# Kernel tuning notes

Measured on AMD Instinct MI355X. Metric: run time of the kernel, lower is better.

The kernel has to match this reference:

```python
import jax, jax.numpy as jnp
import numpy as np
from jax import lax

B, N, D = 4, 64, 32  # graphs, nodes/graph, volume side
HC = 1024            # hidden_channels
NF = 2048            # num_node_features = 32*(D//8)**3
NC = 4               # num_classes
LC = 256             # linear_channels = N*(HC//4)//64


def setup_inputs() -> dict:
    key = jax.random.key(0)
    ks = jax.random.split(key, 16)
    x = jax.random.normal(ks[0], (B, N, D, D, D), jnp.float32)
    # binary symmetric adjacency, zero diagonal (edge presence only; GCNConv ignores values)
    u = jax.random.uniform(ks[1], (B, N, N))
    a = (u < 0.2).astype(jnp.int32)
    a = jnp.maximum(a, a.transpose(0, 2, 1)) * (1 - jnp.eye(N, dtype=jnp.int32))
    s = 0.05
    inp = dict(
        x=x, adj=a, batch_size=B,
        w_conv1=jax.random.normal(ks[2], (16, 1, 3, 3, 3), jnp.float32) * s,
        b_conv1=jnp.zeros((16,), jnp.float32),
        w_conv2=jax.random.normal(ks[3], (32, 16, 3, 3, 3), jnp.float32) * s,
        b_conv2=jnp.zeros((32,), jnp.float32),
        w_g1=jax.random.normal(ks[4], (NF, HC), jnp.float32) * s,
        b_g1=jnp.zeros((HC,), jnp.float32),
        w_g2=jax.random.normal(ks[5], (HC, HC // 2), jnp.float32) * s,
        b_g2=jnp.zeros((HC // 2,), jnp.float32),
        w_g3=jax.random.normal(ks[6], (HC // 2, HC // 4), jnp.float32) * s,
        b_g3=jnp.zeros((HC // 4,), jnp.float32),
        w_fc1=jax.random.normal(ks[7], (LC, 2 * LC), jnp.float32) * s,
        b_fc1=jnp.zeros((2 * LC,), jnp.float32),
        w_fc2=jax.random.normal(ks[8], (2 * LC, NC), jnp.float32) * s,
        b_fc2=jnp.zeros((NC,), jnp.float32),
    )
    return inp


DN = ('NCDHW', 'OIDHW', 'NCDHW')


def _maxpool3(h):
    # MaxPool3d(kernel=3, stride=2, padding=1); pad value -inf matches torch
    return lax.reduce_window(h, -jnp.inf, lax.max,
                             (1, 1, 3, 3, 3), (1, 1, 2, 2, 2),
                             [(0, 0), (0, 0), (1, 1), (1, 1), (1, 1)])


def _gcn_norm(adj, dtype):
    # GCNConv: A_hat = A + I, sym-normalized D^-1/2 A_hat D^-1/2 (per graph)
    A = (adj != 0).astype(dtype) + jnp.eye(adj.shape[-1], dtype=dtype)[None]
    deg = A.sum(-1)                        # [B, N], >= 1
    dinv = deg ** -0.5
    return A * dinv[:, :, None] * dinv[:, None, :]


def _forward(x, adj, batch_size, w_conv1, b_conv1, w_conv2, b_conv2,
             w_g1, b_g1, w_g2, b_g2, w_g3, b_g3, w_fc1, b_fc1, w_fc2, b_fc2):
    b, n = x.shape[0], x.shape[1]
    v = x.reshape(b * n, 1, x.shape[2], x.shape[3], x.shape[4])
    h = lax.conv_general_dilated(v, w_conv1, (1, 1, 1), [(1, 1)] * 3, dimension_numbers=DN)
    h = jax.nn.relu(h + b_conv1[None, :, None, None, None])
    h = _maxpool3(h)                                     # [BN,16,16,16,16]
    h = lax.conv_general_dilated(h, w_conv2, (2, 2, 2), [(1, 1)] * 3, dimension_numbers=DN)
    h = jax.nn.relu(h + b_conv2[None, :, None, None, None])
    h = _maxpool3(h)                                     # [BN,32,4,4,4]
    feat = h.reshape(b, n, -1)                           # [B,N,2048]

    A_norm = _gcn_norm(adj, feat.dtype)                  # [B,N,N]
    gcn = lambda X, W, bb: jnp.einsum('bij,bjf->bif', A_norm, X @ W) + bb
    g = jax.nn.relu(gcn(feat, w_g1, b_g1))
    g = jax.nn.relu(gcn(g, w_g2, b_g2))
    g = gcn(g, w_g3, b_g3)                               # [B,N,256] (no relu, matches source)

    g = g.reshape(batch_size, -1)                        # [B, 16384]
    g = g.reshape(batch_size, -1, 64).max(-1)            # MaxPool1d(64) on 2D input -> [B,256]
    g = jax.nn.relu(g @ w_fc1 + b_fc1)
    return jax.nn.softmax(g @ w_fc2 + b_fc2, axis=-1)


def reference(x, adj, batch_size, w_conv1, b_conv1, w_conv2, b_conv2,
              w_g1, b_g1, w_g2, b_g2, w_g3, b_g3, w_fc1, b_fc1, w_fc2, b_fc2):
    return _forward(x, adj, batch_size, w_conv1, b_conv1, w_conv2, b_conv2,
                    w_g1, b_g1, w_g2, b_g2, w_g3, b_g3, w_fc1, b_fc1, w_fc2, b_fc2)
```

## Files before the change

kernel.cpp:

```cpp
#include <hip/hip_runtime.h>

typedef unsigned short ushort_t;
typedef unsigned long long ull_t;
typedef __attribute__((ext_vector_type(8))) short bf16x8;
typedef __attribute__((ext_vector_type(4))) float f32x4;

static __device__ __forceinline__ unsigned short f2bf(float f) {
  unsigned u = __float_as_uint(f);
  u = (u + 0x7FFFu + ((u >> 16) & 1u)) >> 16;
  return (unsigned short)u;
}

static __device__ __forceinline__ f32x4 max4(f32x4 a, f32x4 b) {
  f32x4 r;
  r[0] = fmaxf(a[0], b[0]); r[1] = fmaxf(a[1], b[1]);
  r[2] = fmaxf(a[2], b[2]); r[3] = fmaxf(a[3], b[3]);
  return r;
}


__device__ __forceinline__ void prep_transpose(
    const float* __restrict__ W, ushort_t* __restrict__ out,
    int K, int N, int n0, int k0, int t, float (*tile)[33])
{
  const int tx = t & 31, ty = t >> 5;
#pragma unroll
  for (int i = 0; i < 4; ++i) {
    const int k = k0 + ty + i * 8;
    tile[ty + i * 8][tx] = W[(size_t)k * N + n0 + tx];
  }
  __syncthreads();
#pragma unroll
  for (int i = 0; i < 4; ++i) {
    const int n = n0 + ty + i * 8;
    out[(size_t)n * K + k0 + tx] = f2bf(tile[tx][ty + i * 8]);
  }
}

__global__ __launch_bounds__(256) void k_prep(
    const float* __restrict__ x, ushort_t* __restrict__ xb16,
    const float* __restrict__ w2, ushort_t* __restrict__ w2f,
    const float* __restrict__ wg1, ushort_t* __restrict__ wg1T,
    const float* __restrict__ wg2, ushort_t* __restrict__ wg2T,
    const float* __restrict__ wg3, ushort_t* __restrict__ wg3T,
    const int* __restrict__ adj, float* __restrict__ An)
{
  __shared__ float tile[32][33];
  __shared__ float dinv[64];
  __shared__ int part[256];
  int b = blockIdx.x;
  const int t = threadIdx.x;
  if (b < 8192) {
    const int tid = b * 256 + t;
    const float4 v = ((const float4*)x)[tid];
    const unsigned lo = (unsigned)f2bf(v.x) | ((unsigned)f2bf(v.y) << 16);
    const unsigned hi = (unsigned)f2bf(v.z) | ((unsigned)f2bf(v.w) << 16);
    ((uint2*)xb16)[tid] = make_uint2(lo, hi);
    return;
  }
  b -= 8192;
  if (b < 56) {
    const int tid = b * 256 + t;
    if (tid < 14336) {
      const int nt = tid / 7168, rem = tid % 7168;
      const int kk = rem / 512, rem2 = rem % 512;
      const int l = rem2 >> 3, j = rem2 & 7;
      const int n = nt * 16 + (l & 15);
      const int k = (l >> 4) * 8 + kk * 32 + j;
      float v = 0.f;
      if (k < 432) v = w2[n * 432 + k];
      w2f[tid] = f2bf(v);
    }
    return;
  }
  b -= 56;
  if (b < 2048) { prep_transpose(wg1, wg1T, 2048, 1024, (b & 31) << 5, (b >> 5) << 5, t, tile); return; }
  b -= 2048;
  if (b < 512)  { prep_transpose(wg2, wg2T, 1024, 512,  (b & 15) << 5, (b >> 4) << 5, t, tile); return; }
  b -= 512;
  if (b < 128)  { prep_transpose(wg3, wg3T, 512,  256,  (b & 7)  << 5, (b >> 3) << 5, t, tile); return; }
  b -= 128;
  {
    const int i = t >> 2, q = t & 3;
    const int* ab = adj + b * 4096 + i * 64 + q * 16;
    int d = 0;
#pragma unroll
    for (int j = 0; j < 16; ++j) d += (ab[j] != 0) ? 1 : 0;
    part[t] = d;
    __syncthreads();
    if (q == 0)
      dinv[i] = rsqrtf((float)(1 + part[t] + part[t + 1] + part[t + 2] + part[t + 3]));
    __syncthreads();
    for (int idx = t; idx < 4096; idx += 256) {
      const int ii = idx >> 6, jj = idx & 63;
      const float a = (ii == jj) ? 1.f : ((adj[b * 4096 + idx] != 0) ? 1.f : 0.f);
      An[b * 4096 + idx] = a * dinv[ii] * dinv[jj];
    }
  }
}

__global__ __launch_bounds__(256) void k_conv1_mfma(
    const ushort_t* __restrict__ xb16, const float* __restrict__ wc,
    const float* __restrict__ bc, ushort_t* __restrict__ h1)
{
  __shared__ ushort_t L[2 * 34 * 76];
  char* Lb = (char*)L;
  const int bn = blockIdx.x >> 3, zg = blockIdx.x & 7;
  const int t = threadIdx.x;
  const int w = t >> 6, l = t & 63;
  const int grp = l >> 4, m = l & 15, ch = l & 15;
  const float NINF = -1e30f;

  union { short s[8]; bf16x8 v; } uA, uB;
#pragma unroll
  for (int j = 0; j < 8; ++j) {
    const int k = grp * 8 + j;
    float wA = 0.f, wB = 0.f;
    if (k < 12) {
      const int dx = k >> 2, dz = k & 3;
      if (dz < 3) { wA = wc[ch*27 + dz*9 + 0 + dx]; wB = wc[ch*27 + dz*9 + 6 + dx]; }
    } else if (k >= 16 && k < 28) {
      const int kk = k - 16, dx = kk >> 2, dz = kk & 3;
      if (dz < 3) wA = wc[ch*27 + dz*9 + 3 + dx];
    }
    uA.s[j] = (short)f2bf(wA);
    uB.s[j] = (short)f2bf(wB);
  }

  int aX1[3], aX2[3];
#pragma unroll
  for (int s = 0; s < 3; ++s) {
    const int Q1 = 2*m + s + 2*(grp & 1);
    const int Q2 = Q1 + 1;
    aX1[s] = (Q1 & 1) * 5168 + (Q1 >> 1) * 8;
    aX2[s] = (Q2 & 1) * 5168 + (Q2 >> 1) * 8;
  }
  const int rsel = (grp >> 1) * 152;

  for (int u = t; u < 200; u += 256) {
    int addr;
    if (u < 72) {
      const int rr = (u < 36) ? 0 : 33;
      const int s = (u < 36) ? u : u - 36;
      const int pp = s / 18, slot = s - pp * 18;
      addr = pp * 5168 + rr * 152 + slot * 8;
    } else {
      const int v = u - 72;
      const int rr = 1 + (v >> 2);
      const int pp = (v >> 1) & 1;
      const int slot = (v & 1) * 17;
      addr = pp * 5168 + rr * 152 + slot * 8;
    }
    *(ull_t*)(Lb + addr) = 0ull;
  }

  f32x4 accZ[4][2];
#pragma unroll
  for (int j = 0; j < 4; ++j)
#pragma unroll
    for (int p = 0; p < 2; ++p) accZ[j][p] = (f32x4){NINF, NINF, NINF, NINF};

  const ushort_t* xb = xb16 + (size_t)bn * 32768;

#pragma unroll 1
  for (int ci = 0; ci < 5; ++ci) {
    const int cz = 4*zg - 1 + ci;
    if (cz < 0) continue;
    if (t < 128) {
      const int r = 1 + (t >> 2), g = t & 3;
      const ushort_t* xrow = xb + (r - 1) * 32 + g * 8;
      uint4 u0 = make_uint4(0u, 0u, 0u, 0u), u2 = make_uint4(0u, 0u, 0u, 0u);
      if (cz > 0)  u0 = *(const uint4*)(xrow + (cz - 1) * 1024);
      const uint4 u1 = *(const uint4*)(xrow + cz * 1024);
      if (cz < 31) u2 = *(const uint4*)(xrow + (cz + 1) * 1024);
      char* b0 = Lb + r * 152 + (4 * g + 1) * 8;
      char* b1 = Lb + 5168 + r * 152 + (4 * g + 1) * 8;
      const unsigned* p0 = (const unsigned*)&u0;
      const unsigned* p1 = (const unsigned*)&u1;
      const unsigned* p2 = (const unsigned*)&u2;
#pragma unroll
      for (int e = 0; e < 4; ++e) {
        const unsigned w0 = p0[e], w1 = p1[e], w2v = p2[e];
        const unsigned lo_e = (w0 & 0xFFFFu) | (w1 << 16);
        const unsigned hi_e = (w2v & 0xFFFFu);
        const unsigned lo_o = (w0 >> 16) | (w1 & 0xFFFF0000u);
        const unsigned hi_o = (w2v >> 16);
        *(ull_t*)(b0 + e * 8) = (ull_t)lo_e | ((ull_t)hi_e << 32);
        *(ull_t*)(b1 + e * 8) = (ull_t)lo_o | ((ull_t)hi_o << 32);
      }
    }
    __syncthreads();
    f32x4 accP0 = (f32x4){NINF, NINF, NINF, NINF};
    f32x4 accP1 = (f32x4){NINF, NINF, NINF, NINF};
#pragma unroll
    for (int yy = 0; yy < 9; ++yy) {
      if (yy == 0 && w == 0) continue;
      const int y = 8 * w - 1 + yy;
      const int rbA = y * 152 + rsel;
      const int rbB = (y + 2) * 152;
      f32x4 Cy;
#pragma unroll
      for (int s = 0; s < 3; ++s) {
        union { ull_t u[2]; bf16x8 v; } fA, fB;
        fA.u[0] = *(const ull_t*)(Lb + aX1[s] + rbA);
        fA.u[1] = *(const ull_t*)(Lb + aX2[s] + rbA);
        fB.u[0] = *(const ull_t*)(Lb + aX1[s] + rbB);
        fB.u[1] = *(const ull_t*)(Lb + aX2[s] + rbB);
        f32x4 acc = (f32x4){0.f, 0.f, 0.f, 0.f};
        acc = __builtin_amdgcn_mfma_f32_16x16x32_bf16(fA.v, uA.v, acc, 0, 0, 0);
        acc = __builtin_amdgcn_mfma_f32_16x16x32_bf16(fB.v, uB.v, acc, 0, 0, 0);
        if (s == 0) acc[0] = (l < 16) ? NINF : acc[0];
        Cy = (s == 0) ? acc : max4(Cy, acc);
      }
      if (yy & 1) {
        const int c = (yy - 1) / 2;
        if ((c & 1) == 0) accP0 = max4(accP0, Cy); else accP1 = max4(accP1, Cy);
      } else {
        const int cl = yy / 2 - 1;
        const int chh = yy / 2;
        if (cl >= 0) {
          if ((cl & 1) == 0) {
            accP0 = max4(accP0, Cy);
            if (ci <= 2) accZ[cl][0] = max4(accZ[cl][0], accP0);
            if (ci >= 2) accZ[cl][1] = max4(accZ[cl][1], accP0);
            accP0 = (f32x4){NINF, NINF, NINF, NINF};
          } else {
            accP1 = max4(accP1, Cy);
            if (ci <= 2) accZ[cl][0] = max4(accZ[cl][0], accP1);
            if (ci >= 2) accZ[cl][1] = max4(accZ[cl][1], accP1);
            accP1 = (f32x4){NINF, NINF, NINF, NINF};
          }
        }
        if (chh <= 3) {
          if ((chh & 1) == 0) accP0 = max4(accP0, Cy); else accP1 = max4(accP1, Cy);
        }
      }
    }
    __syncthreads();
  }

  const float biasv = bc[ch];
#pragma unroll
  for (int j = 0; j < 4; ++j) {
    const int py = 4 * w + j;
#pragma unroll
    for (int p = 0; p < 2; ++p) {
      const int pz = 2 * zg + p;
      const f32x4 v = accZ[j][p];
      const unsigned lo = (unsigned)f2bf(fmaxf(v[0] + biasv, 0.f)) |
                          ((unsigned)f2bf(fmaxf(v[1] + biasv, 0.f)) << 16);
      const unsigned hi = (unsigned)f2bf(fmaxf(v[2] + biasv, 0.f)) |
                          ((unsigned)f2bf(fmaxf(v[3] + biasv, 0.f)) << 16);
      ushort_t* dst = h1 + (((size_t)(bn * 16 + ch) * 16 + pz) << 8) + py * 16 + grp * 4;
      *(uint2*)dst = make_uint2(lo, hi);
    }
  }
}

__global__ __launch_bounds__(128) void k_conv2(
    const ushort_t* __restrict__ h1, const ushort_t* __restrict__ w2f,
    float* __restrict__ c2)
{
  __shared__ ushort_t U[16 * 456];
  ushort_t* Hs = U;
  unsigned* Hsd = (unsigned*)U;
  ushort_t* As = U;
  const int b = blockIdx.x;
  const int bn = b >> 5, oz = (b >> 2) & 7, yg = b & 3;
  const int t = threadIdx.x;
  const ushort_t* hb = h1 + ((size_t)bn << 16);
  const int w = t >> 6, l = t & 63;

  bf16x8 bfr[14];
#pragma unroll
  for (int kk = 0; kk < 14; ++kk)
    bfr[kk] = *(const bf16x8*)(const void*)&w2f[(((w * 14) + kk) * 64 + l) * 8];

#pragma unroll
  for (int it = 0; it < 9; ++it) {
    const int u = t + it * 128;
    const int row = u >> 2, q = u & 3;
    const int ic = row / 18;
    const int r2 = row - ic * 18;
    const int izp = r2 / 6;
    const int iyp = r2 - izp * 6;
    const int iz = 2 * oz - 1 + izp;
    const int iy = 4 * yg - 1 + iyp;
    uint2 v = make_uint2(0u, 0u);
    if ((unsigned)iz < 16u && (unsigned)iy < 16u)
      v = *(const uint2*)(hb + (ic << 12) + (iz << 8) + (iy << 4) + q * 4);
    *(uint2*)&Hs[row * 20 + q * 4] = v;
  }
  __syncthreads();

  const int m = t >> 3, sub = t & 7;
  const int ox = m & 7;
  const int my = (m >> 3) * 2;
  ushort_t tv[54];
  int j = 0;
#pragma unroll
  for (int ic2 = 0; ic2 < 2; ++ic2) {
    const int ic = sub * 2 + ic2;
#pragma unroll
    for (int dz = 0; dz < 3; ++dz) {
#pragma unroll
      for (int dy = 0; dy < 3; ++dy) {
        const int row = ic * 18 + dz * 6 + my + dy;
        const unsigned* rp = Hsd + row * 10;
        const unsigned d0 = (ox > 0) ? rp[ox - 1] : 0u;
        const unsigned d1 = rp[ox];
        tv[j]     = (ushort_t)(d0 >> 16);
        tv[j + 1] = (ushort_t)(d1 & 0xFFFFu);
        tv[j + 2] = (ushort_t)(d1 >> 16);
        j += 3;
      }
    }
  }
  __syncthreads();

  {
    unsigned* Aw = (unsigned*)As;
    const int wbase = m * 228 + sub * 27;
#pragma unroll
    for (int p = 0; p < 27; ++p)
      Aw[wbase + p] = (unsigned)tv[2 * p] | ((unsigned)tv[2 * p + 1] << 16);
    Aw[(t >> 3) * 228 + 216 + (t & 7)] = 0u;
  }
  __syncthreads();

  f32x4 acc = {0.f, 0.f, 0.f, 0.f};
  const ushort_t* arow = &As[(l & 15) * 456 + ((l >> 4) << 3)];
#pragma unroll
  for (int kk = 0; kk < 14; ++kk) {
    const bf16x8 af = *(const bf16x8*)(const void*)&arow[kk * 32];
    acc = __builtin_amdgcn_mfma_f32_16x16x32_bf16(af, bfr[kk], acc, 0, 0, 0);
  }
  const int n = w * 16 + (l & 15);
  const int m0 = (l >> 4) << 2;
  float* cb = c2 + (((size_t)(bn * 32 + n) * 8) + oz) * 64 + yg * 16 + m0;
  *(float4*)cb = make_float4(acc[0], acc[1], acc[2], acc[3]);
}

__global__ __launch_bounds__(256) void k_pool2(
    const float* __restrict__ c2, const float* __restrict__ bc2,
    ushort_t* __restrict__ featb)
{
  const int tid = blockIdx.x * 256 + threadIdx.x;
  const int bn = tid >> 9, r = tid & 511;
  const int ch = r >> 4, pz = (r >> 2) & 3, py = r & 3;
  const float* base = c2 + ((size_t)(bn * 32 + ch) << 9);
  float m0 = -1e30f, m1 = -1e30f, m2 = -1e30f, m3 = -1e30f;
#pragma unroll
  for (int dz = 0; dz < 3; ++dz) {
    const int oz = 2 * pz - 1 + dz;
    if ((unsigned)oz >= 8u) continue;
#pragma unroll
    for (int dy = 0; dy < 3; ++dy) {
      const int oy = 2 * py - 1 + dy;
      if ((unsigned)oy >= 8u) continue;
      const float* row = base + (oz << 6) + (oy << 3);
      const float4 a = ((const float4*)row)[0];
      const float4 b = ((const float4*)row)[1];
      m0 = fmaxf(m0, fmaxf(a.x, a.y));
      m1 = fmaxf(m1, fmaxf(a.y, fmaxf(a.z, a.w)));
      m2 = fmaxf(m2, fmaxf(a.w, fmaxf(b.x, b.y)));
      m3 = fmaxf(m3, fmaxf(b.y, fmaxf(b.z, b.w)));
    }
  }
  const float bb = bc2[ch];
  const unsigned lo = (unsigned)f2bf(fmaxf(m0 + bb, 0.f)) |
                      ((unsigned)f2bf(fmaxf(m1 + bb, 0.f)) << 16);
  const unsigned hi = (unsigned)f2bf(fmaxf(m2 + bb, 0.f)) |
                      ((unsigned)f2bf(fmaxf(m3 + bb, 0.f)) << 16);
  *(uint2*)(featb + (size_t)bn * 2048 + r * 4) = make_uint2(lo, hi);
}

__global__ __launch_bounds__(256) void k_gcn_layer(
    const ushort_t* __restrict__ Xb, const ushort_t* __restrict__ WT,
    const float* __restrict__ bias, const float* __restrict__ An,
    ushort_t* __restrict__ Ob, float* __restrict__ Of, int K, int N, int relu)
{
  __shared__ ushort_t As[2][64 * 72];
  __shared__ ushort_t Bs[2][64 * 72];
  __shared__ ushort_t Ps[64 * 72];
  const int b = blockIdx.y, jb = blockIdx.x << 6;
  const int t = threadIdx.x, w = t >> 6, l = t & 63;
  const int r0 = t >> 3, kc0 = t & 7;
  const int lm = l & 15, lg = l >> 4;

  union { short s[8]; bf16x8 v; } afr[2];
  {
    const float* ap = An + b * 4096 + (16 * w + lm) * 64 + (lg << 3);
#pragma unroll
    for (int kc = 0; kc < 2; ++kc) {
      const float4 v0 = *(const float4*)(ap + kc * 32);
      const float4 v1 = *(const float4*)(ap + kc * 32 + 4);
      afr[kc].s[0] = (short)f2bf(v0.x); afr[kc].s[1] = (short)f2bf(v0.y);
      afr[kc].s[2] = (short)f2bf(v0.z); afr[kc].s[3] = (short)f2bf(v0.w);
      afr[kc].s[4] = (short)f2bf(v1.x); afr[kc].s[5] = (short)f2bf(v1.y);
      afr[kc].s[6] = (short)f2bf(v1.z); afr[kc].s[7] = (short)f2bf(v1.w);
    }
  }

  f32x4 acc[4];
#pragma unroll
  for (int nt = 0; nt < 4; ++nt) acc[nt] = (f32x4){0.f, 0.f, 0.f, 0.f};

  const ushort_t* arow0 = &Xb[(size_t)(b * 64 + r0) * K + kc0 * 8];
  const ushort_t* arow1 = &Xb[(size_t)(b * 64 + r0 + 32) * K + kc0 * 8];
  const ushort_t* brow0 = &WT[(size_t)(jb + r0) * K + kc0 * 8];
  const ushort_t* brow1 = &WT[(size_t)(jb + r0 + 32) * K + kc0 * 8];

  uint4 va0 = *(const uint4*)arow0;
  uint4 va1 = *(const uint4*)arow1;
  uint4 vb0 = *(const uint4*)brow0;
  uint4 vb1 = *(const uint4*)brow1;

  int buf = 0;
#pragma unroll 1
  for (int kt = 0; kt < K; kt += 64) {
    *(uint4*)&As[buf][r0 * 72 + kc0 * 8]        = va0;
    *(uint4*)&As[buf][(r0 + 32) * 72 + kc0 * 8] = va1;
    *(uint4*)&Bs[buf][r0 * 72 + kc0 * 8]        = vb0;
    *(uint4*)&Bs[buf][(r0 + 32) * 72 + kc0 * 8] = vb1;
    __syncthreads();
    if (kt + 64 < K) {
      va0 = *(const uint4*)(arow0 + kt + 64);
      va1 = *(const uint4*)(arow1 + kt + 64);
      vb0 = *(const uint4*)(brow0 + kt + 64);
      vb1 = *(const uint4*)(brow1 + kt + 64);
    }
#pragma unroll
    for (int ks = 0; ks < 2; ++ks) {
      const bf16x8 af = *(const bf16x8*)(const void*)
          &As[buf][(16 * w + lm) * 72 + ks * 32 + (lg << 3)];
#pragma unroll
      for (int nt = 0; nt < 4; ++nt) {
        const bf16x8 bf = *(const bf16x8*)(const void*)
            &Bs[buf][(nt * 16 + lm) * 72 + ks * 32 + (lg << 3)];
        acc[nt] = __builtin_amdgcn_mfma_f32_16x16x32_bf16(af, bf, acc[nt], 0, 0, 0);
      }
    }
    buf ^= 1;
  }

  __syncthreads();
  const int m0 = lg << 2;
#pragma unroll
  for (int nt = 0; nt < 4; ++nt) {
    const int n = nt * 16 + lm;
    const unsigned lo = (unsigned)f2bf(acc[nt][0]) | ((unsigned)f2bf(acc[nt][1]) << 16);
    const unsigned hi = (unsigned)f2bf(acc[nt][2]) | ((unsigned)f2bf(acc[nt][3]) << 16);
    *(uint2*)&Ps[n * 72 + 16 * w + m0] = make_uint2(lo, hi);
  }
  __syncthreads();

#pragma unroll
  for (int nt = 0; nt < 4; ++nt) {
    const bf16x8 b0 = *(const bf16x8*)(const void*)&Ps[(nt * 16 + lm) * 72 + (lg << 3)];
    const bf16x8 b1 = *(const bf16x8*)(const void*)&Ps[(nt * 16 + lm) * 72 + 32 + (lg << 3)];
    f32x4 a2 = (f32x4){0.f, 0.f, 0.f, 0.f};
    a2 = __builtin_amdgcn_mfma_f32_16x16x32_bf16(afr[0].v, b0, a2, 0, 0, 0);
    a2 = __builtin_amdgcn_mfma_f32_16x16x32_bf16(afr[1].v, b1, a2, 0, 0, 0);
    const int col = jb + nt * 16 + lm;
    const float bv = bias[col];
#pragma unroll
    for (int r = 0; r < 4; ++r) {
      const int row = b * 64 + 16 * w + m0 + r;
      float v = a2[r] + bv;
      if (relu) v = fmaxf(v, 0.f);
      if (Ob) Ob[(size_t)row * N + col] = f2bf(v);
      else    Of[(size_t)row * N + col] = v;
    }
  }
}

__global__ __launch_bounds__(256) void k_head(
    const float* __restrict__ g3, const float* __restrict__ w1, const float* __restrict__ b1,
    const float* __restrict__ w2, const float* __restrict__ b2, float* __restrict__ out)
{
  const int b = blockIdx.x, t = threadIdx.x;
  __shared__ float sp[256];
  __shared__ float sh[512];
  __shared__ float sl[4];
  {
    const int n = t >> 2, c = t & 3;
    const float* gr = g3 + (size_t)(b * 64 + n) * 256 + c * 64;
    float mx = -1e30f;
    for (int f = 0; f < 64; ++f) mx = fmaxf(mx, gr[f]);
    sp[t] = mx;
  }
  __syncthreads();
  for (int jj = t; jj < 512; jj += 256) {
    float s = b1[jj];
    for (int k = 0; k < 256; ++k) s += sp[k] * w1[k * 512 + jj];
    sh[jj] = fmaxf(s, 0.f);
  }
  __syncthreads();
  if (t < 4) {
    float s = b2[t];
    for (int k = 0; k < 512; ++k) s += sh[k] * w2[k * 4 + t];
    sl[t] = s;
  }
  __syncthreads();
  if (t == 0) {
    const float mm = fmaxf(fmaxf(sl[0], sl[1]), fmaxf(sl[2], sl[3]));
    const float e0 = expf(sl[0] - mm), e1 = expf(sl[1] - mm);
    const float e2 = expf(sl[2] - mm), e3 = expf(sl[3] - mm);
    const float inv = 1.f / (e0 + e1 + e2 + e3);
    out[b * 4 + 0] = e0 * inv;
    out[b * 4 + 1] = e1 * inv;
    out[b * 4 + 2] = e2 * inv;
    out[b * 4 + 3] = e3 * inv;
  }
}

extern "C" void kernel_launch(void* const* d_in, const int* in_sizes, int n_in,
                              void* d_out, int out_size, void* d_ws, size_t ws_size,
                              hipStream_t stream)
{
  (void)in_sizes; (void)n_in; (void)out_size; (void)ws_size;
  const float* x   = (const float*)d_in[0];
  const int*   adj = (const int*)d_in[1];
  const float* wc1 = (const float*)d_in[3];
  const float* bc1 = (const float*)d_in[4];
  const float* wc2 = (const float*)d_in[5];
  const float* bc2 = (const float*)d_in[6];
  const float* wg1 = (const float*)d_in[7];
  const float* bg1 = (const float*)d_in[8];
  const float* wg2 = (const float*)d_in[9];
  const float* bg2 = (const float*)d_in[10];
  const float* wg3 = (const float*)d_in[11];
  const float* bg3 = (const float*)d_in[12];
  const float* wf1 = (const float*)d_in[13];
  const float* bf1 = (const float*)d_in[14];
  const float* wf2 = (const float*)d_in[15];
  const float* bf2 = (const float*)d_in[16];

  float* ws    = (float*)d_ws;
  ushort_t* h1 = (ushort_t*)d_ws;
  ushort_t* w2f   = (ushort_t*)(ws + 8388608);
  ushort_t* wg1Tb = (ushort_t*)(ws + 8395776);
  ushort_t* wg2Tb = (ushort_t*)(ws + 9444352);
  ushort_t* wg3Tb = (ushort_t*)(ws + 9706496);
  ushort_t* featb = (ushort_t*)(ws + 9772032);
  ushort_t* g1b   = (ushort_t*)(ws + 10034176);
  ushort_t* g2b   = (ushort_t*)(ws + 10165248);
  float* c2    = ws + 16777216;
  ushort_t* xb16 = (ushort_t*)(ws + 16777216);
  float* An   = ws + 21495808;
  float* g3   = ws + 22364160;
  float* outp = (float*)d_out;

  hipLaunchKernelGGL(k_prep,        dim3(10940),    dim3(256), 0, stream,
                     x, xb16, wc2, w2f, wg1, wg1Tb, wg2, wg2Tb, wg3, wg3Tb, adj, An);
  hipLaunchKernelGGL(k_conv1_mfma,  dim3(2048),     dim3(256), 0, stream, xb16, wc1, bc1, h1);
  hipLaunchKernelGGL(k_conv2,       dim3(8192),     dim3(128), 0, stream, h1, w2f, c2);
  hipLaunchKernelGGL(k_pool2,       dim3(512),      dim3(256), 0, stream, c2, bc2, featb);
  hipLaunchKernelGGL(k_gcn_layer,   dim3(16,4),     dim3(256), 0, stream,
                     featb, wg1Tb, bg1, An, g1b, (float*)nullptr, 2048, 1024, 1);
  hipLaunchKernelGGL(k_gcn_layer,   dim3(8,4),      dim3(256), 0, stream,
                     g1b, wg2Tb, bg2, An, g2b, (float*)nullptr, 1024, 512, 1);
  hipLaunchKernelGGL(k_gcn_layer,   dim3(4,4),      dim3(256), 0, stream,
                     g2b, wg3Tb, bg3, An, (ushort_t*)nullptr, g3, 512, 256, 0);
  hipLaunchKernelGGL(k_head,        dim3(4),        dim3(256), 0, stream, g3, wf1, bf1, wf2, bf2, outp);
}
```

Measured before the change: 268.9 us.

## Fuse GCN layers and head into one persistent kernel with grid barriers

```diff
diff --git a/kernel.cpp b/kernel.cpp
--- a/kernel.cpp
+++ b/kernel.cpp
@@ -16,6 +16,26 @@
   r[0] = fmaxf(a[0], b[0]); r[1] = fmaxf(a[1], b[1]);
   r[2] = fmaxf(a[2], b[2]); r[3] = fmaxf(a[3], b[3]);
   return r;
+}
+
+static __device__ __forceinline__ void gbar(int* bar, int nb) {
+  __syncthreads();
+  if (threadIdx.x == 0) {
+    const int g = atomicAdd(&bar[1], 0);
+    __threadfence();
+    if (atomicAdd(&bar[0], 1) == nb - 1) {
+      atomicExch(&bar[0], 0);
+      __threadfence();
+      atomicAdd(&bar[1], 1);
+    } else {
+      for (int it = 0; it < (1 << 24); ++it) {
+        if (atomicAdd(&bar[1], 0) != g) break;
+        __builtin_amdgcn_s_sleep(8);
+      }
+    }
+    __threadfence();
+  }
+  __syncthreads();
 }
 
 
@@ -343,8 +363,9 @@
 
 __global__ __launch_bounds__(256) void k_pool2(
     const float* __restrict__ c2, const float* __restrict__ bc2,
-    ushort_t* __restrict__ featb)
-{
+    ushort_t* __restrict__ featb, int* __restrict__ bar)
+{
+  if (blockIdx.x == 0 && threadIdx.x == 0) { bar[0] = 0; bar[1] = 0; }
   const int tid = blockIdx.x * 256 + threadIdx.x;
   const int bn = tid >> 9, r = tid & 511;
   const int ch = r >> 4, pz = (r >> 2) & 3, py = r & 3;
@@ -375,15 +396,13 @@
   *(uint2*)(featb + (size_t)bn * 2048 + r * 4) = make_uint2(lo, hi);
 }
 
-__global__ __launch_bounds__(256) void k_gcn_layer(
+__device__ __forceinline__ void gcn_body(
     const ushort_t* __restrict__ Xb, const ushort_t* __restrict__ WT,
     const float* __restrict__ bias, const float* __restrict__ An,
-    ushort_t* __restrict__ Ob, float* __restrict__ Of, int K, int N, int relu)
-{
-  __shared__ ushort_t As[2][64 * 72];
-  __shared__ ushort_t Bs[2][64 * 72];
-  __shared__ ushort_t Ps[64 * 72];
-  const int b = blockIdx.y, jb = blockIdx.x << 6;
+    ushort_t* __restrict__ Ob, float* __restrict__ spw,
+    int K, int N, int relu, int b, int jb,
+    ushort_t (*As)[64 * 72], ushort_t (*Bs)[64 * 72], ushort_t* Ps)
+{
   const int t = threadIdx.x, w = t >> 6, l = t & 63;
   const int r0 = t >> 3, kc0 = t & 7;
   const int lm = l & 15, lg = l >> 4;
@@ -455,6 +474,7 @@
   }
   __syncthreads();
 
+  float mx0 = -1e30f, mx1 = -1e30f, mx2 = -1e30f, mx3 = -1e30f;
 #pragma unroll
   for (int nt = 0; nt < 4; ++nt) {
     const bf16x8 b0 = *(const bf16x8*)(const void*)&Ps[(nt * 16 + lm) * 72 + (lg << 3)];
@@ -464,54 +484,126 @@
     a2 = __builtin_amdgcn_mfma_f32_16x16x32_bf16(afr[1].v, b1, a2, 0, 0, 0);
     const int col = jb + nt * 16 + lm;
     const float bv = bias[col];
-#pragma unroll
-    for (int r = 0; r < 4; ++r) {
-      const int row = b * 64 + 16 * w + m0 + r;
-      float v = a2[r] + bv;
-      if (relu) v = fmaxf(v, 0.f);
-      if (Ob) Ob[(size_t)row * N + col] = f2bf(v);
-      else    Of[(size_t)row * N + col] = v;
-    }
-  }
-}
-
-__global__ __launch_bounds__(256) void k_head(
-    const float* __restrict__ g3, const float* __restrict__ w1, const float* __restrict__ b1,
-    const float* __restrict__ w2, const float* __restrict__ b2, float* __restrict__ out)
-{
-  const int b = blockIdx.x, t = threadIdx.x;
-  __shared__ float sp[256];
-  __shared__ float sh[512];
-  __shared__ float sl[4];
+    if (spw) {
+      mx0 = fmaxf(mx0, a2[0] + bv);
+      mx1 = fmaxf(mx1, a2[1] + bv);
+      mx2 = fmaxf(mx2, a2[2] + bv);
+      mx3 = fmaxf(mx3, a2[3] + bv);
+    } else {
+#pragma unroll
+      for (int r = 0; r < 4; ++r) {
+        const int row = b * 64 + 16 * w + m0 + r;
+        float v = a2[r] + bv;
+        if (relu) v = fmaxf(v, 0.f);
+        Ob[(size_t)row * N + col] = f2bf(v);
+      }
+    }
+  }
+  if (spw) {
+#pragma unroll
+    for (int mk = 1; mk <= 8; mk <<= 1) {
+      mx0 = fmaxf(mx0, __shfl_xor(mx0, mk));
+      mx1 = fmaxf(mx1, __shfl_xor(mx1, mk));
+      mx2 = fmaxf(mx2, __shfl_xor(mx2, mk));
+      mx3 = fmaxf(mx3, __shfl_xor(mx3, mk));
+    }
+    if (lm == 0) {
+      const int c = jb >> 6;
+      const int n = 16 * w + m0;
+      spw[b * 256 + (n + 0) * 4 + c] = mx0;
+      spw[b * 256 + (n + 1) * 4 + c] = mx1;
+      spw[b * 256 + (n + 2) * 4 + c] = mx2;
+      spw[b * 256 + (n + 3) * 4 + c] = mx3;
+    }
+  }
+}
+
+__global__ __launch_bounds__(256) void k_tail(
+    const ushort_t* __restrict__ featb,
+    const ushort_t* __restrict__ wg1T, const float* __restrict__ bg1,
+    const ushort_t* __restrict__ wg2T, const float* __restrict__ bg2,
+    const ushort_t* __restrict__ wg3T, const float* __restrict__ bg3,
+    const float* __restrict__ An,
+    ushort_t* __restrict__ g1b, ushort_t* __restrict__ g2b,
+    float* __restrict__ spw, float* __restrict__ shw,
+    const float* __restrict__ w1, const float* __restrict__ b1,
+    const float* __restrict__ w2, const float* __restrict__ b2,
+    float* __restrict__ out, int* __restrict__ bar)
+{
+  __shared__ ushort_t As[2][64 * 72];
+  __shared__ ushort_t Bs[2][64 * 72];
+  __shared__ ushort_t Ps[64 * 72];
+  __shared__ float red[260];
+  const int bx = blockIdx.x, t = threadIdx.x;
+
+  gcn_body(featb, wg1T, bg1, An, g1b, nullptr, 2048, 1024, 1,
+           bx >> 4, (bx & 15) << 6, As, Bs, Ps);
+  gbar(bar, 64);
+
+  if (bx < 32)
+    gcn_body(g1b, wg2T, bg2, An, g2b, nullptr, 1024, 512, 1,
+             bx >> 3, (bx & 7) << 6, As, Bs, Ps);
+  gbar(bar, 64);
+
+  if (bx < 16)
+    gcn_body(g2b, wg3T, bg3, An, nullptr, spw, 512, 256, 0,
+             bx >> 2, (bx & 3) << 6, As, Bs, Ps);
+  gbar(bar, 64);
+
   {
-    const int n = t >> 2, c = t & 3;
-    const float* gr = g3 + (size_t)(b * 64 + n) * 256 + c * 64;
-    float mx = -1e30f;
-    for (int f = 0; f < 64; ++f) mx = fmaxf(mx, gr[f]);
-    sp[t] = mx;
-  }
-  __syncthreads();
-  for (int jj = t; jj < 512; jj += 256) {
-    float s = b1[jj];
-    for (int k = 0; k < 256; ++k) s += sp[k] * w1[k * 512 + jj];
-    sh[jj] = fmaxf(s, 0.f);
-  }
-  __syncthreads();
-  if (t < 4) {
-    float s = b2[t];
-    for (int k = 0; k < 512; ++k) s += sh[k] * w2[k * 4 + t];
-    sl[t] = s;
-  }
-  __syncthreads();
-  if (t == 0) {
-    const float mm = fmaxf(fmaxf(sl[0], sl[1]), fmaxf(sl[2], sl[3]));
-    const float e0 = expf(sl[0] - mm), e1 = expf(sl[1] - mm);
-    const float e2 = expf(sl[2] - mm), e3 = expf(sl[3] - mm);
-    const float inv = 1.f / (e0 + e1 + e2 + e3);
-    out[b * 4 + 0] = e0 * inv;
-    out[b * 4 + 1] = e1 * inv;
-    out[b * 4 + 2] = e2 * inv;
-    out[b * 4 + 3] = e3 * inv;
+    const int oo = t & 31, ks = t >> 5;
+    const int bb = bx >> 4;
+    const int jj = (bx & 15) * 32 + oo;
+    const float* spb = spw + bb * 256;
+    float s = 0.f;
+#pragma unroll
+    for (int i = 0; i < 32; ++i) {
+      const int k = ks * 32 + i;
+      s += spb[k] * w1[k * 512 + jj];
+    }
+    red[t] = s;
+    __syncthreads();
+    if (t < 32) {
+      float s2 = 0.f;
+#pragma unroll
+      for (int i = 0; i < 8; ++i) s2 += red[t + i * 32];
+      const int j2 = (bx & 15) * 32 + t;
+      shw[bb * 512 + j2] = fmaxf(s2 + b1[j2], 0.f);
+    }
+  }
+  gbar(bar, 64);
+
+  if (bx < 4) {
+    float s = 0.f;
+    if (t < 128) {
+      const int c = t & 3, ks2 = t >> 2;
+      const float* shb = shw + bx * 512;
+#pragma unroll
+      for (int i = 0; i < 16; ++i) {
+        const int k = ks2 * 16 + i;
+        s += shb[k] * w2[k * 4 + c];
+      }
+    }
+    red[t] = s;
+    __syncthreads();
+    if (t < 4) {
+      float s2 = b2[t];
+#pragma unroll
+      for (int i = 0; i < 32; ++i) s2 += red[t + i * 4];
+      red[256 + t] = s2;
+    }
+    __syncthreads();
+    if (t == 0) {
+      const float a0 = red[256], a1 = red[257], a2v = red[258], a3 = red[259];
+      const float mm = fmaxf(fmaxf(a0, a1), fmaxf(a2v, a3));
+      const float e0 = expf(a0 - mm), e1 = expf(a1 - mm);
+      const float e2 = expf(a2v - mm), e3 = expf(a3 - mm);
+      const float inv = 1.f / (e0 + e1 + e2 + e3);
+      out[bx * 4 + 0] = e0 * inv;
+      out[bx * 4 + 1] = e1 * inv;
+      out[bx * 4 + 2] = e2 * inv;
+      out[bx * 4 + 3] = e3 * inv;
+    }
   }
 }
 
@@ -549,19 +641,17 @@
   float* c2    = ws + 16777216;
   ushort_t* xb16 = (ushort_t*)(ws + 16777216);
   float* An   = ws + 21495808;
-  float* g3   = ws + 22364160;
+  float* spw  = ws + 10034176;
+  float* shw  = ws + 10035200;
+  int*   bar  = (int*)(ws + 22364160);
   float* outp = (float*)d_out;
 
   hipLaunchKernelGGL(k_prep,        dim3(10940),    dim3(256), 0, stream,
                      x, xb16, wc2, w2f, wg1, wg1Tb, wg2, wg2Tb, wg3, wg3Tb, adj, An);
   hipLaunchKernelGGL(k_conv1_mfma,  dim3(2048),     dim3(256), 0, stream, xb16, wc1, bc1, h1);
   hipLaunchKernelGGL(k_conv2,       dim3(8192),     dim3(128), 0, stream, h1, w2f, c2);
-  hipLaunchKernelGGL(k_pool2,       dim3(512),      dim3(256), 0, stream, c2, bc2, featb);
-  hipLaunchKernelGGL(k_gcn_layer,   dim3(16,4),     dim3(256), 0, stream,
-                     featb, wg1Tb, bg1, An, g1b, (float*)nullptr, 2048, 1024, 1);
-  hipLaunchKernelGGL(k_gcn_layer,   dim3(8,4),      dim3(256), 0, stream,
-                     g1b, wg2Tb, bg2, An, g2b, (float*)nullptr, 1024, 512, 1);
-  hipLaunchKernelGGL(k_gcn_layer,   dim3(4,4),      dim3(256), 0, stream,
-                     g2b, wg3Tb, bg3, An, (ushort_t*)nullptr, g3, 512, 256, 0);
-  hipLaunchKernelGGL(k_head,        dim3(4),        dim3(256), 0, stream, g3, wf1, bf1, wf2, bf2, outp);
-}
+  hipLaunchKernelGGL(k_pool2,       dim3(512),      dim3(256), 0, stream, c2, bc2, featb, bar);
+  hipLaunchKernelGGL(k_tail,        dim3(64),       dim3(256), 0, stream,
+                     featb, wg1Tb, bg1, wg2Tb, bg2, wg3Tb, bg3, An, g1b, g2b,
+                     spw, shw, wf1, bf1, wf2, bf2, outp, bar);
+}
```

New measurement: 249.9 us. 1.08x faster.
